# Kernel optimization log

Measured on AMD Instinct MI355X. Metric: run time of the kernel, lower is better.

The kernel has to match this reference:

```python
import jax, jax.numpy as jnp
import numpy as np

D_MODEL = 1024
NUM_HEADS = 16
HEAD_DIM = D_MODEL // NUM_HEADS
B, S = 2, 2048
EPS = 1e-8


def setup_inputs() -> dict:
    key = jax.random.key(0)
    ks = jax.random.split(key, 9)
    sc = 1.0 / np.sqrt(D_MODEL)
    return {
        "x": jax.random.normal(ks[0], (B, S, D_MODEL), jnp.float32),
        "wq": jax.random.normal(ks[1], (D_MODEL, D_MODEL), jnp.float32) * sc,
        "bq": jax.random.normal(ks[2], (D_MODEL,), jnp.float32) * 0.01,
        "wk": jax.random.normal(ks[3], (D_MODEL, D_MODEL), jnp.float32) * sc,
        "bk": jax.random.normal(ks[4], (D_MODEL,), jnp.float32) * 0.01,
        "wv": jax.random.normal(ks[5], (D_MODEL, D_MODEL), jnp.float32) * sc,
        "bv": jax.random.normal(ks[6], (D_MODEL,), jnp.float32) * 0.01,
        "wo": jax.random.normal(ks[7], (D_MODEL, D_MODEL), jnp.float32) * sc,
        "bo": jax.random.normal(ks[8], (D_MODEL,), jnp.float32) * 0.01,
    }


def reference(x, wq, bq, wk, bk, wv, bv, wo, bo):
    b, s, d = x.shape
    h, hd = NUM_HEADS, HEAD_DIM
    # projections (torch Linear: y = x W^T + b); reshape to [b, h, s, hd]
    def proj(w, bias):
        return (jnp.einsum('bsd,ed->bse', x, w) + bias).reshape(b, s, h, hd).transpose(0, 2, 1, 3)
    q = proj(wq, bq)
    k = proj(wk, bk)
    v = proj(wv, bv)
    scores = jnp.einsum('bhqd,bhkd->bhqk', q, k) / np.sqrt(hd)
    attn = jax.nn.softmax(scores, axis=-1)
    o = jnp.einsum('bhqk,bhkd->bhqd', attn, v)  # [b, h, s, hd]
    # per-position, per-head Gram-Schmidt exclusion: remove component of o[i]
    # along v[i] (the loop in the original is independent over positions)
    v_norm_sq = jnp.sum(v * v, axis=-1, keepdims=True)          # [b,h,s,1]
    align = jnp.sum(o * v, axis=-1, keepdims=True) / (v_norm_sq + EPS)
    o = o - align * v
    o = o.transpose(0, 2, 1, 3).reshape(b, s, d)
    return jnp.einsum('bsd,ed->bse', o, wo) + bo
```

## Files before the change

kernel.cpp:

```cpp
#include <hip/hip_runtime.h>
#include <stdint.h>

#define SEQ 2048
#define NTOK 4096
#define DM 1024

typedef __bf16 bf16x8 __attribute__((ext_vector_type(8)));
typedef __bf16 bf16x4 __attribute__((ext_vector_type(4)));
typedef float f32x4 __attribute__((ext_vector_type(4)));

__device__ __forceinline__ unsigned short f2bf(float f) {
  union { float f; unsigned u; } v; v.f = f;
  return (unsigned short)((v.u + 0x7fffu + ((v.u >> 16) & 1u)) >> 16);
}
__device__ __forceinline__ float bf2f(unsigned short s) {
  union { unsigned u; float f; } v; v.u = ((unsigned)s) << 16; return v.f;
}
__device__ __forceinline__ unsigned pkbf(float a, float b) {
  union { float f; unsigned u; } x, y; x.f = a; y.f = b;
  return __builtin_amdgcn_perm(y.u + 0x8000u, x.u + 0x8000u, 0x07060302u);
}

__device__ __forceinline__ void async16(const unsigned short* g, unsigned short* l) {
  __builtin_amdgcn_global_load_lds(
      (const __attribute__((address_space(1))) void*)g,
      (__attribute__((address_space(3))) void*)l, 16, 0, 0);
}

__global__ __launch_bounds__(256) void cast_all(
    const float* __restrict__ x, const float* __restrict__ wq,
    const float* __restrict__ wk, const float* __restrict__ wv,
    const float* __restrict__ wo, unsigned short* __restrict__ dst) {
  size_t i = ((size_t)blockIdx.x * 256 + threadIdx.x) * 4;
  const float* src; size_t off;
  if (i < (size_t)NTOK * DM) { src = x; off = i; }
  else {
    size_t j = i - (size_t)NTOK * DM;
    int s = (int)(j >> 20);
    src = (s == 0) ? wq : (s == 1) ? wk : (s == 2) ? wv : wo;
    off = j & 1048575u;
  }
  float4 f = *(const float4*)(src + off);
  ushort4 o;
  o.x = f2bf(f.x); o.y = f2bf(f.y); o.z = f2bf(f.z); o.w = f2bf(f.w);
  *(ushort4*)(dst + i) = o;
}


template<int MI>
__device__ __forceinline__ void stage_half(
    const unsigned short* __restrict__ A, const unsigned short* __restrict__ Bw,
    int m0, int n0, int kt, unsigned short* As, unsigned short* Bs) {
  const int tid = threadIdx.x;
  const int r = tid >> 2, c = tid & 3;
#pragma unroll
  for (int b = 0; b < MI / 2; ++b) {
    const int row = b * 64 + r;
    async16(A + (size_t)(m0 + row) * 1024 + kt + ((c ^ (row & 3)) << 3),
            As + row * 32 + c * 8);
  }
#pragma unroll
  for (int b = 0; b < 2; ++b) {
    const int row = b * 64 + r;
    async16(Bw + (size_t)(n0 + row) * 1024 + kt + ((c ^ (row & 3)) << 3),
            Bs + row * 32 + c * 8);
  }
}

__device__ __forceinline__ void pipe_bar0() {
  asm volatile("s_waitcnt vmcnt(0)\ns_barrier" ::: "memory");
}
template<int MI>
__device__ __forceinline__ void pipe_barN() {
  if constexpr (MI == 4) asm volatile("s_waitcnt vmcnt(4)\ns_barrier" ::: "memory");
  else                   asm volatile("s_waitcnt vmcnt(3)\ns_barrier" ::: "memory");
}

template<int MI>
__device__ __forceinline__ void gemm_pipe(
    const unsigned short* __restrict__ A, const unsigned short* __restrict__ Bw,
    int m0, int n0, f32x4 (&acc)[MI][4],
    unsigned short* AsBase, unsigned short* BsBase) {
  const int tid = threadIdx.x, lane = tid & 63, w = tid >> 6;
  const int wm16 = (w >> 1) * MI * 16, wn = (w & 1) * 64;
  const int quad = lane >> 4, l16 = lane & 15;
  constexpr int ASZ = MI * 32 * 32;
  constexpr int BSZ = 128 * 32;

  stage_half<MI>(A, Bw, m0, n0, 0,  AsBase,       BsBase);
  stage_half<MI>(A, Bw, m0, n0, 32, AsBase + ASZ, BsBase + BSZ);
  pipe_barN<MI>();

  int cur = 0;
  for (int p = 0; p < 32; ++p) {
    const unsigned short* As = AsBase + cur * ASZ;
    const unsigned short* Bs = BsBase + cur * BSZ;

    bf16x8 af[MI], bf[4];
    const int swz = ((quad ^ (l16 & 3)) << 3);
#pragma unroll
    for (int i = 0; i < MI; ++i)
      af[i] = *(const bf16x8*)(As + (wm16 + i * 16 + l16) * 32 + swz);
#pragma unroll
    for (int j = 0; j < 4; ++j)
      bf[j] = *(const bf16x8*)(Bs + (wn + j * 16 + l16) * 32 + swz);

    if (p + 2 < 32) {
      const int slot = (cur == 0) ? 2 : cur - 1;
      stage_half<MI>(A, Bw, m0, n0, (p + 2) * 32,
                     AsBase + slot * ASZ, BsBase + slot * BSZ);
    }

#pragma unroll
    for (int i = 0; i < MI; ++i)
#pragma unroll
      for (int j = 0; j < 4; ++j)
        acc[i][j] = __builtin_amdgcn_mfma_f32_16x16x32_bf16(af[i], bf[j], acc[i][j], 0, 0, 0);

    if (p < 30)       pipe_barN<MI>();
    else if (p == 30) pipe_bar0();
    cur = (cur == 2) ? 0 : cur + 1;
  }
}

__global__ __launch_bounds__(256, 3) void qkv_gemm(
    const unsigned short* __restrict__ xb,
    const unsigned short* __restrict__ wqb, const unsigned short* __restrict__ wkb,
    const unsigned short* __restrict__ wvb,
    const float* __restrict__ bq, const float* __restrict__ bk, const float* __restrict__ bv,
    unsigned short* __restrict__ Q, unsigned short* __restrict__ Kd,
    unsigned short* __restrict__ Vt) {
  __shared__ unsigned short As[3 * 128 * 32], Bs[3 * 128 * 32];
  const int gx = blockIdx.x;
  const int kind = gx >> 8;
  const int rr = gx & 255;
  const int tok = 4 * (rr & 7) + ((rr >> 3) & 3);
  const int oth = rr >> 5;
  const unsigned short* A; const unsigned short* Bw;
  int m0, n0;
  if (kind == 2) { A = wvb; Bw = xb; m0 = oth * 128; n0 = tok * 128; }
  else { A = xb; Bw = kind ? wkb : wqb; m0 = tok * 128; n0 = oth * 128; }

  f32x4 acc[4][4];
#pragma unroll
  for (int i = 0; i < 4; ++i)
#pragma unroll
    for (int j = 0; j < 4; ++j) { f32x4 z = {0.f, 0.f, 0.f, 0.f}; acc[i][j] = z; }
  gemm_pipe<4>(A, Bw, m0, n0, acc, As, Bs);

  const int lane = threadIdx.x & 63, w = threadIdx.x >> 6;
  const int quad = lane >> 4, l16 = lane & 15;
  const int wm = (w >> 1) * 64, wn = (w & 1) * 64;

  if (kind == 2) {
#pragma unroll
    for (int i = 0; i < 4; ++i)
#pragma unroll
      for (int j = 0; j < 4; ++j) {
        const int n = n0 + wn + j * 16 + l16;
        const int tb = n >> 11, s = n & 2047;
#pragma unroll
        for (int r = 0; r < 4; ++r) {
          const int m = m0 + wm + i * 16 + quad * 4 + r;
          const int h = m >> 6, d = m & 63;
          Vt[((size_t)(tb * 16 + h) * 64 + d) * SEQ + s] = f2bf(acc[i][j][r] + bv[m]);
        }
      }
  } else {
    const float* bias = (kind == 0) ? bq : bk;
    const float scale = (kind == 0) ? 0.180336880f : 1.0f;
#pragma unroll
    for (int i = 0; i < 4; ++i)
#pragma unroll
      for (int j = 0; j < 4; ++j) {
        const int col = n0 + wn + j * 16 + l16;
        const float bb = bias[col];
        const int h = col >> 6, d = col & 63;
#pragma unroll
        for (int r = 0; r < 4; ++r) {
          const int m = m0 + wm + i * 16 + quad * 4 + r;
          const int b = m >> 11, s = m & 2047;
          const int bh = b * 16 + h;
          const unsigned short val = f2bf((acc[i][j][r] + bb) * scale);
          if (kind == 0) Q[((size_t)bh * SEQ + s) * 64 + d] = val;
          else           Kd[((size_t)bh * SEQ + s) * 64 + d] = val;
        }
      }
  }
}

__global__ __launch_bounds__(256, 4) void attn_kernel(
    const unsigned short* __restrict__ Q, const unsigned short* __restrict__ Kd,
    const unsigned short* __restrict__ Vt,
    unsigned short* __restrict__ Op, float* __restrict__ Lp) {
  __shared__ unsigned short KV[4][4096];
  const int gx = blockIdx.x;
  const int xcd = gx & 7;
  const int idx = gx >> 3;
  const int bh  = xcd * 4 + (idx & 3);
  const int ksl = (idx >> 2) & 1;
  const int q0  = (idx >> 3) * 128;
  const int ks0 = ksl << 10;
  const int tid = threadIdx.x, lane = tid & 63, w = tid >> 6;
  const int quad = lane >> 4, l16 = lane & 15;
  const unsigned short* Qp = Q + (size_t)bh * SEQ * 64;
  const unsigned short* Kp = Kd + (size_t)bh * SEQ * 64;
  const unsigned short* Vp = Vt + (size_t)bh * 64 * SEQ;
  const int srow = tid >> 3;
  const int sc = ((tid & 7) ^ (srow & 7)) << 3;

#pragma unroll
  for (int c = 0; c < 4; ++c)
    async16(Qp + (size_t)(q0 + c * 32 + srow) * 64 + sc,
            KV[c >> 1] + (c & 1) * 2048 + tid * 8);
  __syncthreads();

  const int sel = l16 & 7;
  const unsigned short* Qsrc = KV[w >> 1] + (w & 1) * 2048;
  bf16x8 bQ[2][2];
#pragma unroll
  for (int qq = 0; qq < 2; ++qq) {
    const int qrow = qq * 16 + l16;
#pragma unroll
    for (int hh = 0; hh < 2; ++hh)
      bQ[qq][hh] = *(const bf16x8*)(Qsrc + qrow * 64 + (((hh * 4 + quad) ^ sel) << 3));
  }
  __syncthreads();

  async16(Kp + (size_t)(ks0 + srow) * 64 + sc, KV[0] + tid * 8);
  async16(Kp + (size_t)(ks0 + 32 + srow) * 64 + sc, KV[0] + 2048 + tid * 8);
  async16(Vp + (size_t)srow * SEQ + ks0 + sc, KV[2] + tid * 8);
  async16(Vp + (size_t)(32 + srow) * SEQ + ks0 + sc, KV[2] + 2048 + tid * 8);

  union { unsigned short u[8]; bf16x8 v; } one8;
#pragma unroll
  for (int t = 0; t < 8; ++t) one8.u[t] = 0x3F80;
  const bf16x8 aOnes = one8.v;

  f32x4 o_acc[2][4];
  f32x4 l_acc[2];
  const f32x4 zinit = {-12.f, -12.f, -12.f, -12.f};
#pragma unroll
  for (int qq = 0; qq < 2; ++qq) {
    f32x4 z = {0.f, 0.f, 0.f, 0.f};
    l_acc[qq] = z;
#pragma unroll
    for (int dt = 0; dt < 4; ++dt) o_acc[qq][dt] = z;
  }

  for (int it = 0; it < 16; ++it) {
    const int cur = it & 1;
    __syncthreads();
    if (it + 1 < 16) {
      const int kt = ks0 + (it + 1) * 64, nb = (it + 1) & 1;
      async16(Kp + (size_t)(kt + srow) * 64 + sc, KV[nb] + tid * 8);
      async16(Kp + (size_t)(kt + 32 + srow) * 64 + sc, KV[nb] + 2048 + tid * 8);
      async16(Vp + (size_t)srow * SEQ + kt + sc, KV[2 + nb] + tid * 8);
      async16(Vp + (size_t)(32 + srow) * SEQ + kt + sc, KV[2 + nb] + 2048 + tid * 8);
    }
    const unsigned short* Ks = KV[cur];
    const unsigned short* Vs = KV[2 + cur];

    bf16x8 bP[2][2];
#pragma unroll
    for (int kk = 0; kk < 4; ++kk) {
      const int krow = kk * 16 + l16;
      bf16x8 a0 = *(const bf16x8*)(Ks + krow * 64 + ((quad ^ sel) << 3));
      bf16x8 a1 = *(const bf16x8*)(Ks + krow * 64 + (((4 + quad) ^ sel) << 3));
#pragma unroll
      for (int qq = 0; qq < 2; ++qq) {
        f32x4 z = __builtin_amdgcn_mfma_f32_16x16x32_bf16(a0, bQ[qq][0], zinit, 0, 0, 0);
        z = __builtin_amdgcn_mfma_f32_16x16x32_bf16(a1, bQ[qq][1], z, 0, 0, 0);
#pragma unroll
        for (int r = 0; r < 4; ++r) z[r] = __builtin_amdgcn_exp2f(z[r]);
        unsigned lo = pkbf(z[0], z[1]);
        unsigned hi = pkbf(z[2], z[3]);
        union { unsigned d[4]; bf16x8 v; } pk;
        pk.v = bP[qq][kk >> 1];
        pk.d[(kk & 1) * 2] = lo;
        pk.d[(kk & 1) * 2 + 1] = hi;
        bP[qq][kk >> 1] = pk.v;
      }
    }

#pragma unroll
    for (int qq = 0; qq < 2; ++qq)
#pragma unroll
      for (int G = 0; G < 2; ++G)
        l_acc[qq] = __builtin_amdgcn_mfma_f32_16x16x32_bf16(aOnes, bP[qq][G], l_acc[qq], 0, 0, 0);

#pragma unroll
    for (int dt = 0; dt < 4; ++dt) {
      const unsigned short* vbase = Vs + (dt * 16 + l16) * 64;
      const int inner = (quad & 1) * 4;
#pragma unroll
      for (int G = 0; G < 2; ++G) {
        const int c0 = 4 * G + (quad >> 1);
        bf16x4 lo = *(const bf16x4*)(vbase + ((c0 ^ sel) << 3) + inner);
        bf16x4 hi = *(const bf16x4*)(vbase + (((c0 + 2) ^ sel) << 3) + inner);
        bf16x8 aV = __builtin_shufflevector(lo, hi, 0, 1, 2, 3, 4, 5, 6, 7);
#pragma unroll
        for (int qq = 0; qq < 2; ++qq)
          o_acc[qq][dt] = __builtin_amdgcn_mfma_f32_16x16x32_bf16(aV, bP[qq][G], o_acc[qq][dt], 0, 0, 0);
      }
    }
  }

  const size_t sb = (size_t)(ksl * 32 + bh);
#pragma unroll
  for (int qq = 0; qq < 2; ++qq) {
    const int qg = q0 + w * 32 + qq * 16 + l16;
#pragma unroll
    for (int dt = 0; dt < 4; ++dt)
#pragma unroll
      for (int r = 0; r < 4; ++r) {
        const int d = dt * 16 + quad * 4 + r;
        Op[(sb * 64 + d) * SEQ + qg] = f2bf(o_acc[qq][dt][r]);
      }
    if (quad == 0) Lp[sb * SEQ + qg] = l_acc[qq][0];
  }
}

__global__ __launch_bounds__(128) void combine_kernel(
    const unsigned short* __restrict__ Op, const float* __restrict__ Lp,
    const unsigned short* __restrict__ Vt, unsigned short* __restrict__ O) {
  const int bh = blockIdx.y;
  const int q = blockIdx.x * 128 + threadIdx.x;
  const size_t QC = (size_t)32 * SEQ;
  const size_t idx = (size_t)bh * SEQ + q;
  const float inv = 1.0f / (Lp[idx] + Lp[QC + idx]);
  const unsigned short* O1 = Op + (size_t)bh * 64 * SEQ + q;
  const unsigned short* O2 = O1 + QC * 64;
  const unsigned short* Vp = Vt + (size_t)bh * 64 * SEQ + q;
  float o64[64];
  float ov = 0.f, vv = 0.f;
#pragma unroll
  for (int d = 0; d < 64; ++d) {
    const float o = (bf2f(O1[(size_t)d * SEQ]) + bf2f(O2[(size_t)d * SEQ])) * inv;
    const float v = bf2f(Vp[(size_t)d * SEQ]);
    o64[d] = o; ov += o * v; vv += v * v;
  }
  const float align = ov / (vv + 1e-8f);
  const int b = bh >> 4, h = bh & 15;
  unsigned short* dst = O + (size_t)(b * SEQ + q) * DM + h * 64;
#pragma unroll
  for (int d = 0; d < 64; d += 2) {
    const float a0 = o64[d]     - align * bf2f(Vp[(size_t)d * SEQ]);
    const float a1 = o64[d + 1] - align * bf2f(Vp[(size_t)(d + 1) * SEQ]);
    *(unsigned*)(dst + d) = pkbf(a0, a1);
  }
}

__global__ __launch_bounds__(256) void out_gemm(
    const unsigned short* __restrict__ Ob, const unsigned short* __restrict__ wob,
    const float* __restrict__ bo, float* __restrict__ out) {
  __shared__ unsigned short As[3 * 64 * 32], Bs[3 * 128 * 32];
  const int m0 = blockIdx.y * 64, n0 = blockIdx.x * 128;
  f32x4 acc[2][4];
#pragma unroll
  for (int i = 0; i < 2; ++i)
#pragma unroll
    for (int j = 0; j < 4; ++j) { f32x4 z = {0.f, 0.f, 0.f, 0.f}; acc[i][j] = z; }

  gemm_pipe<2>(Ob, wob, m0, n0, acc, As, Bs);

  const int lane = threadIdx.x & 63, w = threadIdx.x >> 6;
  const int quad = lane >> 4, l16 = lane & 15;
  const int wm = (w >> 1) * 32, wn = (w & 1) * 64;
#pragma unroll
  for (int i = 0; i < 2; ++i)
#pragma unroll
    for (int j = 0; j < 4; ++j) {
      const int col = n0 + wn + j * 16 + l16;
      const float bb = bo[col];
#pragma unroll
      for (int r = 0; r < 4; ++r) {
        const int m = m0 + wm + i * 16 + quad * 4 + r;
        out[(size_t)m * DM + col] = acc[i][j][r] + bb;
      }
    }
}

extern "C" void kernel_launch(void* const* d_in, const int* in_sizes, int n_in,
                              void* d_out, int out_size, void* d_ws, size_t ws_size,
                              hipStream_t stream) {
  const float* x  = (const float*)d_in[0];
  const float* wq = (const float*)d_in[1];
  const float* bq = (const float*)d_in[2];
  const float* wk = (const float*)d_in[3];
  const float* bk = (const float*)d_in[4];
  const float* wv = (const float*)d_in[5];
  const float* bv = (const float*)d_in[6];
  const float* wo = (const float*)d_in[7];
  const float* bo = (const float*)d_in[8];
  float* out = (float*)d_out;
  (void)in_sizes; (void)n_in; (void)out_size; (void)ws_size;

  unsigned short* ws  = (unsigned short*)d_ws;
  unsigned short* xb  = ws;
  unsigned short* wqb = xb + (size_t)NTOK * DM;
  unsigned short* wkb = wqb + (size_t)DM * DM;
  unsigned short* wvb = wkb + (size_t)DM * DM;
  unsigned short* wob = wvb + (size_t)DM * DM;
  unsigned short* Qb  = wob + (size_t)DM * DM;
  unsigned short* Kb  = Qb + (size_t)NTOK * DM;
  unsigned short* Vtb = Kb + (size_t)NTOK * DM;
  unsigned short* Ob  = Vtb + (size_t)NTOK * DM;
  unsigned short* Opb = Ob + (size_t)NTOK * DM;
  float* Lpw = (float*)(Opb + (size_t)2 * 32 * 64 * SEQ);

  cast_all<<<8192, 256, 0, stream>>>(x, wq, wk, wv, wo, ws);
  qkv_gemm<<<768, 256, 0, stream>>>(xb, wqb, wkb, wvb, bq, bk, bv, Qb, Kb, Vtb);
  attn_kernel<<<1024, 256, 0, stream>>>(Qb, Kb, Vtb, Opb, Lpw);
  combine_kernel<<<dim3(16, 32), 128, 0, stream>>>(Opb, Lpw, Vtb, Ob);
  out_gemm<<<dim3(8, 64), 256, 0, stream>>>(Ob, wob, bo, out);
}
```

Baseline: 192.3 us.

## Permute K rows to enable 16-byte V loads and use bit-trick exp2

Reorders which K rows each lane handles during the score MFMA, so the packed P fragments line up with contiguous 8-element V chunks. The V operand can then be read with a single 16-byte LDS load per MFMA instead of two 8-byte loads and a shuffle. The LDS swizzle pattern is changed to match. The hardware exp2 is replaced by a Schraudolph-style float-to-int FMA that builds the bf16 bits directly, cutting transcendental work at the cost of extra approximation error in the softmax weights.

```diff
diff --git a/kernel.cpp b/kernel.cpp
--- a/kernel.cpp
+++ b/kernel.cpp
@@ -207,7 +207,7 @@
   const unsigned short* Kp = Kd + (size_t)bh * SEQ * 64;
   const unsigned short* Vp = Vt + (size_t)bh * 64 * SEQ;
   const int srow = tid >> 3;
-  const int sc = ((tid & 7) ^ (srow & 7)) << 3;
+  const int sc = ((tid & 7) ^ ((srow & 3) | ((srow & 8) >> 1))) << 3;
 
 #pragma unroll
   for (int c = 0; c < 4; ++c)
@@ -215,6 +215,7 @@
             KV[c >> 1] + (c & 1) * 2048 + tid * 8);
   __syncthreads();
 
+  const int gl = (l16 & 3) | ((l16 & 8) >> 1);
   const int sel = l16 & 7;
   const unsigned short* Qsrc = KV[w >> 1] + (w & 1) * 2048;
   bf16x8 bQ[2][2];
@@ -223,7 +224,7 @@
     const int qrow = qq * 16 + l16;
 #pragma unroll
     for (int hh = 0; hh < 2; ++hh)
-      bQ[qq][hh] = *(const bf16x8*)(Qsrc + qrow * 64 + (((hh * 4 + quad) ^ sel) << 3));
+      bQ[qq][hh] = *(const bf16x8*)(Qsrc + qrow * 64 + (((hh * 4 + quad) ^ gl) << 3));
   }
   __syncthreads();
 
@@ -263,23 +264,25 @@
 
     bf16x8 bP[2][2];
 #pragma unroll
-    for (int kk = 0; kk < 4; ++kk) {
-      const int krow = kk * 16 + l16;
-      bf16x8 a0 = *(const bf16x8*)(Ks + krow * 64 + ((quad ^ sel) << 3));
-      bf16x8 a1 = *(const bf16x8*)(Ks + krow * 64 + (((4 + quad) ^ sel) << 3));
+    for (int ee = 0; ee < 4; ++ee) {
+      const int G = ee >> 1, e = ee & 1;
+      const int R = G * 32 + ((l16 >> 2) << 3) + e * 4 + (l16 & 3);
+      const unsigned short* arow = Ks + R * 64;
+      bf16x8 a0 = *(const bf16x8*)(arow + ((quad ^ sel) << 3));
+      bf16x8 a1 = *(const bf16x8*)(arow + (((4 + quad) ^ sel) << 3));
 #pragma unroll
       for (int qq = 0; qq < 2; ++qq) {
         f32x4 z = __builtin_amdgcn_mfma_f32_16x16x32_bf16(a0, bQ[qq][0], zinit, 0, 0, 0);
         z = __builtin_amdgcn_mfma_f32_16x16x32_bf16(a1, bQ[qq][1], z, 0, 0, 0);
-#pragma unroll
-        for (int r = 0; r < 4; ++r) z[r] = __builtin_amdgcn_exp2f(z[r]);
-        unsigned lo = pkbf(z[0], z[1]);
-        unsigned hi = pkbf(z[2], z[3]);
+        const unsigned u0 = (unsigned)(int)__builtin_fmaf(z[0], 8388608.0f, 1065024977.0f);
+        const unsigned u1 = (unsigned)(int)__builtin_fmaf(z[1], 8388608.0f, 1065024977.0f);
+        const unsigned u2 = (unsigned)(int)__builtin_fmaf(z[2], 8388608.0f, 1065024977.0f);
+        const unsigned u3 = (unsigned)(int)__builtin_fmaf(z[3], 8388608.0f, 1065024977.0f);
         union { unsigned d[4]; bf16x8 v; } pk;
-        pk.v = bP[qq][kk >> 1];
-        pk.d[(kk & 1) * 2] = lo;
-        pk.d[(kk & 1) * 2 + 1] = hi;
-        bP[qq][kk >> 1] = pk.v;
+        pk.v = bP[qq][G];
+        pk.d[e * 2]     = __builtin_amdgcn_perm(u1, u0, 0x07060302u);
+        pk.d[e * 2 + 1] = __builtin_amdgcn_perm(u3, u2, 0x07060302u);
+        bP[qq][G] = pk.v;
       }
     }
 
@@ -292,13 +295,9 @@
 #pragma unroll
     for (int dt = 0; dt < 4; ++dt) {
       const unsigned short* vbase = Vs + (dt * 16 + l16) * 64;
-      const int inner = (quad & 1) * 4;
 #pragma unroll
       for (int G = 0; G < 2; ++G) {
-        const int c0 = 4 * G + (quad >> 1);
-        bf16x4 lo = *(const bf16x4*)(vbase + ((c0 ^ sel) << 3) + inner);
-        bf16x4 hi = *(const bf16x4*)(vbase + (((c0 + 2) ^ sel) << 3) + inner);
-        bf16x8 aV = __builtin_shufflevector(lo, hi, 0, 1, 2, 3, 4, 5, 6, 7);
+        bf16x8 aV = *(const bf16x8*)(vbase + (((G * 4 + quad) ^ gl) << 3));
 #pragma unroll
         for (int qq = 0; qq < 2; ++qq)
           o_acc[qq][dt] = __builtin_amdgcn_mfma_f32_16x16x32_bf16(aV, bP[qq][G], o_acc[qq][dt], 0, 0, 0);
```

Measured after the change: 187.7 us. 2.4% less time.
